# Kernel optimization log

Measured on AMD Instinct MI355X. Metric: run time of the kernel, lower is better.

Reference implementation:

```python
import jax, jax.numpy as jnp
import numpy as np

B, C, H, W = 2, 64, 64, 64
DH = C // 2  # 32, projected channel dim

def setup_inputs() -> dict:
    key = jax.random.key(0)
    ks = jax.random.split(key, 9)
    x = jax.random.normal(ks[0], (B, C, H, W), dtype=jnp.float32)
    # 1x1 conv weights stored as [out_ch, in_ch] (kernel dims squeezed)
    w1 = jax.random.normal(ks[1], (DH, C), dtype=jnp.float32) * 0.05
    b1 = jax.random.normal(ks[2], (DH,), dtype=jnp.float32) * 0.05
    w2 = jax.random.normal(ks[3], (DH, C), dtype=jnp.float32) * 0.05
    b2 = jax.random.normal(ks[4], (DH,), dtype=jnp.float32) * 0.05
    w3 = jax.random.normal(ks[5], (DH, C), dtype=jnp.float32) * 0.05
    b3 = jax.random.normal(ks[6], (DH,), dtype=jnp.float32) * 0.05
    w4 = jax.random.normal(ks[7], (C, DH), dtype=jnp.float32) * 0.05
    b4 = jax.random.normal(ks[8], (C,), dtype=jnp.float32) * 0.05
    return {"x": x, "w1": w1, "b1": b1, "w2": w2, "b2": b2,
            "w3": w3, "b3": b3, "w4": w4, "b4": b4}

def _proj(x, w, b):
    # 1x1 conv then permute(0,2,3,1) then flatten(B,H,W) -> [N, DH]
    y = jnp.einsum('bchw,oc->bhwo', x, w) + b
    return y.reshape(-1, w.shape[0])

def reference(x, w1, b1, w2, b2, w3, b3, w4, b4):
    b_, c_, h_, w_ = x.shape
    q = _proj(x, w1, b1)   # [N, DH]
    k = _proj(x, w2, b2)   # [N, DH]
    v = _proj(x, w3, b3)   # [N, DH]
    att = q @ k.T                       # [N, N]
    att = jax.nn.softmax(att, axis=0)   # softmax over dim 0 (rows, per column)
    o = att @ v                         # [N, DH]
    o = o.reshape(b_, h_, w_, c_ // 2)
    # conv4 (1x1) on [B, DH, H, W] then residual
    y = jnp.einsum('bhwc,oc->bohw', o, w4) + b4[None, :, None, None]
    return y + x
```

## Files before the change

### kernel.cpp

```cpp
#include <hip/hip_runtime.h>
#include <hip/hip_bf16.h>

#define N_TOK   8192
#define DH      32
#define CCH     64
#define HWSZ    4096
#define LOG2E   1.4426950408889634f
#define NCH_Z   32
#define NCH_O   32
#define ITILE   128

typedef __attribute__((ext_vector_type(8))) short  bf16x8;
typedef __attribute__((ext_vector_type(4))) short  bf16x4;
typedef __attribute__((ext_vector_type(4))) float  f32x4;

static __device__ __forceinline__ short f2bf(float f) {
    __hip_bfloat16 h = __float2bfloat16(f);
    return __builtin_bit_cast(short, h);
}
static __device__ __forceinline__ float bf2f(short s) {
    unsigned u = ((unsigned)(unsigned short)s) << 16;
    return __builtin_bit_cast(float, u);
}

static __device__ __forceinline__ bf16x8 load_frag8(const __hip_bfloat16* __restrict__ base,
                                                    int row0, int l) {
    const __hip_bfloat16* p = base + (size_t)(row0 + (l & 15)) * DH + ((l >> 4) << 3);
    return *reinterpret_cast<const bf16x8*>(p);
}

__global__ __launch_bounds__(256) void k_qkv(
        const float* __restrict__ x,
        const float* __restrict__ w1, const float* __restrict__ b1,
        const float* __restrict__ w2, const float* __restrict__ b2,
        const float* __restrict__ w3, const float* __restrict__ b3,
        __hip_bfloat16* __restrict__ Qb, __hip_bfloat16* __restrict__ Kb,
        __hip_bfloat16* __restrict__ VTb) {
    __shared__ float4 w1s[16][32];
    __shared__ float4 w2s[16][32];
    __shared__ float4 w3s[16][32];
    __shared__ short  vt[32][8];
    int t = threadIdx.x;
    for (int i = t; i < 512; i += 256) {
        int cg = i >> 5, d = i & 31;
        w1s[cg][d] = *reinterpret_cast<const float4*>(w1 + d * CCH + cg * 4);
        w2s[cg][d] = *reinterpret_cast<const float4*>(w2 + d * CCH + cg * 4);
        w3s[cg][d] = *reinterpret_cast<const float4*>(w3 + d * CCH + cg * 4);
    }
    __syncthreads();
    int d = t & 31, nr = t >> 5;
    int n0 = blockIdx.x * 8;
    int n = n0 + nr;
    int b = n >> 12, hw = n & 4095;
    const float* xp = x + (size_t)b * (CCH * HWSZ) + hw;
    float aq = b1[d], ak = b2[d], av = b3[d];
    #pragma unroll
    for (int cg = 0; cg < 16; ++cg) {
        float x0 = xp[(cg * 4 + 0) * HWSZ];
        float x1 = xp[(cg * 4 + 1) * HWSZ];
        float x2 = xp[(cg * 4 + 2) * HWSZ];
        float x3 = xp[(cg * 4 + 3) * HWSZ];
        float4 a = w1s[cg][d];
        aq = fmaf(a.x, x0, aq); aq = fmaf(a.y, x1, aq);
        aq = fmaf(a.z, x2, aq); aq = fmaf(a.w, x3, aq);
        float4 bb = w2s[cg][d];
        ak = fmaf(bb.x, x0, ak); ak = fmaf(bb.y, x1, ak);
        ak = fmaf(bb.z, x2, ak); ak = fmaf(bb.w, x3, ak);
        float4 cc = w3s[cg][d];
        av = fmaf(cc.x, x0, av); av = fmaf(cc.y, x1, av);
        av = fmaf(cc.z, x2, av); av = fmaf(cc.w, x3, av);
    }
    Qb[(size_t)n * DH + d] = __float2bfloat16(aq * LOG2E);
    Kb[(size_t)n * DH + d] = __float2bfloat16(ak);
    vt[d][nr] = f2bf(av);
    __syncthreads();
    if (t < 32) {
        bf16x8 row = *reinterpret_cast<const bf16x8*>(&vt[t][0]);
        *reinterpret_cast<bf16x8*>(VTb + (size_t)t * N_TOK + n0) = row;
    }
}

__global__ __launch_bounds__(256) void k_z(
        const __hip_bfloat16* __restrict__ Qb, const __hip_bfloat16* __restrict__ Kb,
        float* __restrict__ Zp) {
    int l  = threadIdx.x & 63;
    int gw = blockIdx.x * 4 + (threadIdx.x >> 6);
    int jt = gw >> 5;
    int ic = gw & 31;
    int j0 = jt * 64;
    const int ilen = N_TOK / NCH_Z;
    int i0 = ic * ilen;
    bf16x8 ka[4];
    #pragma unroll
    for (int f = 0; f < 4; ++f) ka[f] = load_frag8(Kb, j0 + f * 16, l);
    float zac[16];
    #pragma unroll
    for (int k = 0; k < 16; ++k) zac[k] = 0.f;
    const f32x4 z4 = {0.f, 0.f, 0.f, 0.f};
    #pragma unroll 2
    for (int i = i0; i < i0 + ilen; i += 16) {
        bf16x8 qf = load_frag8(Qb, i, l);
        #pragma unroll
        for (int f = 0; f < 4; ++f) {
            f32x4 s = __builtin_amdgcn_mfma_f32_16x16x32_bf16(ka[f], qf, z4, 0, 0, 0);
            #pragma unroll
            for (int r = 0; r < 4; ++r)
                zac[f * 4 + r] += __builtin_amdgcn_exp2f(s[r]);
        }
    }
    #pragma unroll
    for (int k = 0; k < 16; ++k) {
        float z = zac[k];
        z += __shfl_xor(z, 1); z += __shfl_xor(z, 2);
        z += __shfl_xor(z, 4); z += __shfl_xor(z, 8);
        zac[k] = z;
    }
    if ((l & 15) == 0) {
        int jr = (l >> 4) * 4;
        #pragma unroll
        for (int f = 0; f < 4; ++f)
            #pragma unroll
            for (int r = 0; r < 4; ++r)
                Zp[(size_t)ic * N_TOK + j0 + f * 16 + jr + r] = zac[f * 4 + r];
    }
}

__global__ __launch_bounds__(256) void k_af(
        const __hip_bfloat16* __restrict__ Qb, const __hip_bfloat16* __restrict__ Kb,
        const __hip_bfloat16* __restrict__ VTb, const float* __restrict__ Zp,
        __hip_bfloat16* __restrict__ oTp) {
    __shared__ float rzs[256];
    int t = threadIdx.x;
    int jc  = blockIdx.x & 31;
    int itg = blockIdx.x >> 5;
    const int jlen = N_TOK / NCH_O;
    int j0c = jc * jlen;
    {
        float z = 0.f;
        #pragma unroll 8
        for (int c = 0; c < NCH_Z; ++c) z += Zp[(size_t)c * N_TOK + j0c + t];
        rzs[t] = __builtin_amdgcn_rcpf(z);
    }
    __syncthreads();
    int l = t & 63;
    int it = itg * 4 + (t >> 6);
    int i0 = it * ITILE;
    bf16x8 qb[8];
    #pragma unroll
    for (int f = 0; f < 8; ++f) qb[f] = load_frag8(Qb, i0 + f * 16, l);
    f32x4 acc0[8], acc1[8];
    #pragma unroll
    for (int f = 0; f < 8; ++f) { acc0[f] = {0.f,0.f,0.f,0.f}; acc1[f] = {0.f,0.f,0.f,0.f}; }
    const f32x4 z4 = {0.f, 0.f, 0.f, 0.f};
    int lo16 = l & 15, hi4 = (l >> 4) << 2;
    const __hip_bfloat16* v0p = VTb + (size_t)lo16 * N_TOK;
    const __hip_bfloat16* v1p = VTb + (size_t)(lo16 + 16) * N_TOK;
    #pragma unroll 2
    for (int jl = 0; jl < jlen; jl += 16) {
        int j = j0c + jl;
        f32x4 rz = *reinterpret_cast<const f32x4*>(&rzs[jl + hi4]);
        bf16x8 kaf = load_frag8(Kb, j, l);
        bf16x4 va0 = *reinterpret_cast<const bf16x4*>(v0p + j + hi4);
        bf16x4 va1 = *reinterpret_cast<const bf16x4*>(v1p + j + hi4);
        #pragma unroll
        for (int f = 0; f < 8; ++f) {
            f32x4 s = __builtin_amdgcn_mfma_f32_16x16x32_bf16(kaf, qb[f], z4, 0, 0, 0);
            bf16x4 e;
            #pragma unroll
            for (int r = 0; r < 4; ++r)
                e[r] = f2bf(__builtin_amdgcn_exp2f(s[r]) * rz[r]);
            acc0[f] = __builtin_amdgcn_mfma_f32_16x16x16bf16_1k(va0, e, acc0[f], 0, 0, 0);
            acc1[f] = __builtin_amdgcn_mfma_f32_16x16x16bf16_1k(va1, e, acc1[f], 0, 0, 0);
        }
    }
    int icol = i0 + lo16;
    #pragma unroll
    for (int f = 0; f < 8; ++f) {
        #pragma unroll
        for (int r = 0; r < 4; ++r) {
            oTp[(size_t)(jc * DH + hi4 + r)      * N_TOK + icol + f * 16] =
                __float2bfloat16(acc0[f][r]);
            oTp[(size_t)(jc * DH + 16 + hi4 + r) * N_TOK + icol + f * 16] =
                __float2bfloat16(acc1[f][r]);
        }
    }
}

__global__ __launch_bounds__(256) void k_fin(
        const __hip_bfloat16* __restrict__ oTp, const float* __restrict__ w4,
        const float* __restrict__ b4, const float* __restrict__ x,
        float* __restrict__ y) {
    __shared__ float w4s[64][32];
    __shared__ float tile[32][36];
    int t = threadIdx.x;
    {
        const float4* w4v = reinterpret_cast<const float4*>(w4);
        float4* dst = reinterpret_cast<float4*>(&w4s[0][0]);
        dst[t * 2]     = w4v[t * 2];
        dst[t * 2 + 1] = w4v[t * 2 + 1];
    }
    int n0 = blockIdx.x * 32;
    int d = t >> 3, seg = t & 7;
    float s[4];
    #pragma unroll
    for (int k = 0; k < 4; ++k) s[k] = 0.f;
    #pragma unroll 4
    for (int c = 0; c < NCH_O; ++c) {
        bf16x4 v = *reinterpret_cast<const bf16x4*>(
            oTp + ((size_t)c * DH + d) * N_TOK + n0 + seg * 4);
        #pragma unroll
        for (int k = 0; k < 4; ++k) s[k] += bf2f(v[k]);
    }
    #pragma unroll
    for (int k = 0; k < 4; ++k) tile[d][seg * 4 + k] = s[k];
    __syncthreads();
    int n_l = t & 31, cgr = t >> 5;
    int n = n0 + n_l, b = n >> 12, hw = n & 4095;
    #pragma unroll
    for (int ci = 0; ci < 8; ++ci) {
        int c = cgr * 8 + ci;
        float acc = b4[c];
        #pragma unroll
        for (int dd = 0; dd < 32; ++dd)
            acc = fmaf(w4s[c][dd], tile[dd][n_l], acc);
        int idx = b * (CCH * HWSZ) + c * HWSZ + hw;
        y[idx] = acc + x[idx];
    }
}

extern "C" void kernel_launch(void* const* d_in, const int* in_sizes, int n_in,
                              void* d_out, int out_size, void* d_ws, size_t ws_size,
                              hipStream_t stream) {
    const float* x  = (const float*)d_in[0];
    const float* w1 = (const float*)d_in[1];
    const float* b1 = (const float*)d_in[2];
    const float* w2 = (const float*)d_in[3];
    const float* b2 = (const float*)d_in[4];
    const float* w3 = (const float*)d_in[5];
    const float* b3 = (const float*)d_in[6];
    const float* w4 = (const float*)d_in[7];
    const float* b4 = (const float*)d_in[8];
    float* y = (float*)d_out;

    char* ws = (char*)d_ws;
    const size_t KB = 1024;
    __hip_bfloat16* Qb  = (__hip_bfloat16*)(ws);
    __hip_bfloat16* Kb  = (__hip_bfloat16*)(ws + 512 * KB);
    __hip_bfloat16* VTb = (__hip_bfloat16*)(ws + 1024 * KB);
    float*          Zp  = (float*)(ws + 1536 * KB);
    __hip_bfloat16* oTp = (__hip_bfloat16*)(ws + 2560 * KB);

    hipLaunchKernelGGL(k_qkv, dim3(N_TOK / 8), dim3(256), 0, stream,
                       x, w1, b1, w2, b2, w3, b3, Qb, Kb, VTb);
    hipLaunchKernelGGL(k_z,   dim3(1024), dim3(256), 0, stream, Qb, Kb, Zp);
    hipLaunchKernelGGL(k_af,  dim3(512),  dim3(256), 0, stream,
                       Qb, Kb, VTb, Zp, oTp);
    hipLaunchKernelGGL(k_fin, dim3(N_TOK / 32), dim3(256), 0, stream,
                       oTp, w4, b4, x, y);
}
```

Before: 66.83 us.

## Stage Q/K/V tiles in shared memory and shrink per-wave tiles in attention kernels

k_z now loads a block's shared 256-row Q chunk into padded LDS once, so the four waves reuse it instead of each reading global memory. k_af stages the K rows and the transposed V slice for its j-chunk into padded LDS. It halves the per-wave i-tile from 128 to 64 and doubles the grid to 1024 blocks to raise parallelism and lower register pressure. Launch bounds ask for 4 blocks per CU. The risks are extra LDS traffic and barrier cost, and the smaller tile means each loaded K/V fragment is reused over fewer MFMAs.

```diff
diff --git a/kernel.cpp b/kernel.cpp
--- a/kernel.cpp
+++ b/kernel.cpp
@@ -8,7 +8,8 @@
 #define LOG2E   1.4426950408889634f
 #define NCH_Z   32
 #define NCH_O   32
-#define ITILE   128
+#define KROW    40
+#define VROW    264
 
 typedef __attribute__((ext_vector_type(8))) short  bf16x8;
 typedef __attribute__((ext_vector_type(4))) short  bf16x4;
@@ -80,16 +81,25 @@
     }
 }
 
-__global__ __launch_bounds__(256) void k_z(
+__global__ __launch_bounds__(256, 4) void k_z(
         const __hip_bfloat16* __restrict__ Qb, const __hip_bfloat16* __restrict__ Kb,
         float* __restrict__ Zp) {
-    int l  = threadIdx.x & 63;
-    int gw = blockIdx.x * 4 + (threadIdx.x >> 6);
-    int jt = gw >> 5;
-    int ic = gw & 31;
-    int j0 = jt * 64;
-    const int ilen = N_TOK / NCH_Z;
-    int i0 = ic * ilen;
+    __shared__ short Qs[256 * KROW];
+    int t = threadIdx.x;
+    int ic  = blockIdx.x & 31;
+    int jtg = blockIdx.x >> 5;
+    int i0c = ic * 256;
+    #pragma unroll
+    for (int p = 0; p < 4; ++p) {
+        int row = p * 64 + (t >> 2), seg = t & 3;
+        bf16x8 v = *reinterpret_cast<const bf16x8*>(
+            Qb + (size_t)(i0c + row) * DH + seg * 8);
+        *reinterpret_cast<bf16x8*>(&Qs[row * KROW + seg * 8]) = v;
+    }
+    __syncthreads();
+    int l = t & 63, w = t >> 6;
+    int lo16 = l & 15, hi = l >> 4;
+    int j0 = (jtg * 4 + w) * 64;
     bf16x8 ka[4];
     #pragma unroll
     for (int f = 0; f < 4; ++f) ka[f] = load_frag8(Kb, j0 + f * 16, l);
@@ -98,8 +108,8 @@
     for (int k = 0; k < 16; ++k) zac[k] = 0.f;
     const f32x4 z4 = {0.f, 0.f, 0.f, 0.f};
     #pragma unroll 2
-    for (int i = i0; i < i0 + ilen; i += 16) {
-        bf16x8 qf = load_frag8(Qb, i, l);
+    for (int il = 0; il < 256; il += 16) {
+        bf16x8 qf = *reinterpret_cast<const bf16x8*>(&Qs[(il + lo16) * KROW + hi * 8]);
         #pragma unroll
         for (int f = 0; f < 4; ++f) {
             f32x4 s = __builtin_amdgcn_mfma_f32_16x16x32_bf16(ka[f], qf, z4, 0, 0, 0);
@@ -125,45 +135,59 @@
     }
 }
 
-__global__ __launch_bounds__(256) void k_af(
+__global__ __launch_bounds__(256, 4) void k_af(
         const __hip_bfloat16* __restrict__ Qb, const __hip_bfloat16* __restrict__ Kb,
         const __hip_bfloat16* __restrict__ VTb, const float* __restrict__ Zp,
         __hip_bfloat16* __restrict__ oTp) {
+    __shared__ short Ks[256 * KROW];
+    __shared__ short Vs[32 * VROW];
     __shared__ float rzs[256];
     int t = threadIdx.x;
     int jc  = blockIdx.x & 31;
     int itg = blockIdx.x >> 5;
-    const int jlen = N_TOK / NCH_O;
-    int j0c = jc * jlen;
+    int j0c = jc * 256;
     {
         float z = 0.f;
         #pragma unroll 8
         for (int c = 0; c < NCH_Z; ++c) z += Zp[(size_t)c * N_TOK + j0c + t];
         rzs[t] = __builtin_amdgcn_rcpf(z);
     }
-    __syncthreads();
-    int l = t & 63;
-    int it = itg * 4 + (t >> 6);
-    int i0 = it * ITILE;
-    bf16x8 qb[8];
-    #pragma unroll
-    for (int f = 0; f < 8; ++f) qb[f] = load_frag8(Qb, i0 + f * 16, l);
-    f32x4 acc0[8], acc1[8];
-    #pragma unroll
-    for (int f = 0; f < 8; ++f) { acc0[f] = {0.f,0.f,0.f,0.f}; acc1[f] = {0.f,0.f,0.f,0.f}; }
+    #pragma unroll
+    for (int p = 0; p < 4; ++p) {
+        int row = p * 64 + (t >> 2), seg = t & 3;
+        bf16x8 v = *reinterpret_cast<const bf16x8*>(
+            Kb + (size_t)(j0c + row) * DH + seg * 8);
+        *reinterpret_cast<bf16x8*>(&Ks[row * KROW + seg * 8]) = v;
+    }
+    {
+        int d = t >> 3, part = t & 7;
+        const __hip_bfloat16* src = VTb + (size_t)d * N_TOK + j0c + part * 32;
+        #pragma unroll
+        for (int q = 0; q < 4; ++q) {
+            bf16x8 v = *reinterpret_cast<const bf16x8*>(src + q * 8);
+            *reinterpret_cast<bf16x8*>(&Vs[d * VROW + part * 32 + q * 8]) = v;
+        }
+    }
+    __syncthreads();
+    int l = t & 63, w = t >> 6;
+    int lo16 = l & 15, hi = l >> 4, hi4 = hi << 2;
+    int it = itg * 4 + w;
+    int i0 = it * 64;
+    bf16x8 qb[4];
+    #pragma unroll
+    for (int f = 0; f < 4; ++f) qb[f] = load_frag8(Qb, i0 + f * 16, l);
+    f32x4 acc0[4], acc1[4];
+    #pragma unroll
+    for (int f = 0; f < 4; ++f) { acc0[f] = {0.f,0.f,0.f,0.f}; acc1[f] = {0.f,0.f,0.f,0.f}; }
     const f32x4 z4 = {0.f, 0.f, 0.f, 0.f};
-    int lo16 = l & 15, hi4 = (l >> 4) << 2;
-    const __hip_bfloat16* v0p = VTb + (size_t)lo16 * N_TOK;
-    const __hip_bfloat16* v1p = VTb + (size_t)(lo16 + 16) * N_TOK;
     #pragma unroll 2
-    for (int jl = 0; jl < jlen; jl += 16) {
-        int j = j0c + jl;
+    for (int jl = 0; jl < 256; jl += 16) {
         f32x4 rz = *reinterpret_cast<const f32x4*>(&rzs[jl + hi4]);
-        bf16x8 kaf = load_frag8(Kb, j, l);
-        bf16x4 va0 = *reinterpret_cast<const bf16x4*>(v0p + j + hi4);
-        bf16x4 va1 = *reinterpret_cast<const bf16x4*>(v1p + j + hi4);
-        #pragma unroll
-        for (int f = 0; f < 8; ++f) {
+        bf16x8 kaf = *reinterpret_cast<const bf16x8*>(&Ks[(jl + lo16) * KROW + hi * 8]);
+        bf16x4 va0 = *reinterpret_cast<const bf16x4*>(&Vs[lo16 * VROW + jl + hi4]);
+        bf16x4 va1 = *reinterpret_cast<const bf16x4*>(&Vs[(lo16 + 16) * VROW + jl + hi4]);
+        #pragma unroll
+        for (int f = 0; f < 4; ++f) {
             f32x4 s = __builtin_amdgcn_mfma_f32_16x16x32_bf16(kaf, qb[f], z4, 0, 0, 0);
             bf16x4 e;
             #pragma unroll
@@ -175,7 +199,7 @@
     }
     int icol = i0 + lo16;
     #pragma unroll
-    for (int f = 0; f < 8; ++f) {
+    for (int f = 0; f < 4; ++f) {
         #pragma unroll
         for (int r = 0; r < 4; ++r) {
             oTp[(size_t)(jc * DH + hi4 + r)      * N_TOK + icol + f * 16] =
@@ -253,7 +277,7 @@
     hipLaunchKernelGGL(k_qkv, dim3(N_TOK / 8), dim3(256), 0, stream,
                        x, w1, b1, w2, b2, w3, b3, Qb, Kb, VTb);
     hipLaunchKernelGGL(k_z,   dim3(1024), dim3(256), 0, stream, Qb, Kb, Zp);
-    hipLaunchKernelGGL(k_af,  dim3(512),  dim3(256), 0, stream,
+    hipLaunchKernelGGL(k_af,  dim3(1024), dim3(256), 0, stream,
                        Qb, Kb, VTb, Zp, oTp);
     hipLaunchKernelGGL(k_fin, dim3(N_TOK / 32), dim3(256), 0, stream,
                        oTp, w4, b4, x, y);
```

Result: faster. 58.00 us (-13.2%).
